# Kernel optimization log

Measured on AMD Instinct MI355X. Metric: run time of the kernel, lower is better.

Reference implementation:

```python
import jax, jax.numpy as jnp
import numpy as np

B, N, C, H = 8, 512, 64, 128
T, K = 10, 2                       # dilation threshold and skip divisor
TAUS = (0.25, 0.5, 0.75)
WTS = (0.25, 0.5, 0.25)
EPS_GIN = 0.0                      # (1 + eps) * x, eps buffer
AVG_DEG = 32.0


def setup_inputs() -> dict:
    key = jax.random.key(0)
    ks = jax.random.split(key, 6)
    x = jax.random.normal(ks[0], (B, N, C), jnp.float32)
    u = jax.random.uniform(ks[1], (B, N, N))
    a = u < (AVG_DEG / N)
    adj = jnp.maximum(a, jnp.swapaxes(a, 1, 2)).astype(jnp.float32)  # symmetric binary adjacency
    mask = jax.random.bernoulli(ks[2], 0.9, (B, N))
    W1 = jax.random.normal(ks[3], (C, H), jnp.float32) / np.float32(np.sqrt(C))
    b1 = jnp.zeros((H,), jnp.float32)
    W2 = jax.random.normal(ks[4], (H, C), jnp.float32) / np.float32(np.sqrt(H))
    b2 = jnp.zeros((C,), jnp.float32)
    return {"x": x, "adj": adj, "mask": mask, "W1": W1, "b1": b1, "W2": W2, "b2": b2}


def reference(x, adj, mask, W1, b1, W2, b2):
    Bc, Nc, Cc = x.shape
    eye = jnp.eye(Nc, dtype=bool)
    adj_ = jnp.where(eye, 1.0, adj)                 # add_loop=True: force self loops
    # ---- vectorized dilation (replaces the per-(b,n) python loop) ----
    neigh = (adj_ > 0) & (~eye)                     # neighbors excluding self [B,N,N]
    ni = neigh.astype(jnp.int32)
    rank = jnp.cumsum(ni, axis=-1) - ni             # exclusive rank of m among n's sorted neighbors
    nb = ni.sum(-1)                                 # [B,N] neighbor count (w/o self)
    skip = jnp.where(nb > T, (nb + K - 1) // K, 1)  # ceil(nb/k) if nb > T else 1 (linear mode, layer 1)
    skip = jnp.maximum(skip, 1)
    sk = skip[:, :, None]
    # remove relative indices skip-1, 2*skip-1, ... when skip > 1, only for masked-in nodes
    rem = neigh & (sk > 1) & ((rank % sk) == (sk - 1)) & mask[:, :, None]
    rem = rem | jnp.swapaxes(rem, 1, 2)             # symmetric removal
    adj_d = jnp.where(rem, 0.0, adj_)
    # ---- masked quantile aggregation over neighbors (== nanquantile) ----
    nd = adj_d > 0                                  # includes self loop -> at least 1 valid
    vals = jnp.where(nd[..., None], x[:, None, :, :], jnp.inf)  # [B,N,M,C]; invalid -> +inf
    s = jnp.sort(vals, axis=2)                      # valid values first, ascending
    nv = nd.sum(2)                                  # [B,N] valid count per node
    agg = jnp.zeros_like(x)
    for tau, w in zip(TAUS, WTS):                   # small fixed loop over quantiles
        pos = jnp.asarray(tau, x.dtype) * jnp.maximum(nv - 1, 0).astype(x.dtype)
        lo = jnp.floor(pos).astype(jnp.int32)
        hi = jnp.ceil(pos).astype(jnp.int32)
        frac = (pos - lo.astype(x.dtype))[..., None]
        idx_lo = jnp.broadcast_to(lo[:, :, None, None], (Bc, Nc, 1, Cc))
        idx_hi = jnp.broadcast_to(hi[:, :, None, None], (Bc, Nc, 1, Cc))
        v_lo = jnp.take_along_axis(s, idx_lo, axis=2)[:, :, 0, :]
        v_hi = jnp.take_along_axis(s, idx_hi, axis=2)[:, :, 0, :]
        agg = agg + jnp.asarray(w, x.dtype) * (v_lo + frac * (v_hi - v_lo))
    agg = jnp.where(nv[..., None] > 0, agg, 0.0)    # nan_to_num for empty rows
    out = (1.0 + EPS_GIN) * x + agg
    h = jax.nn.relu(out @ W1 + b1)                  # GIN MLP: Linear-ReLU-Linear
    y = h @ W2 + b2
    return y * mask[..., None].astype(y.dtype)
```

## Files before the change

kernel.cpp:

```cpp
#include <hip/hip_runtime.h>
#include <cstdint>

#define B_ 8
#define N_ 512
#define C_ 64
#define H_ 128
#define T_ 10
#define K_ 2
#define WPR 16
#define NVMAX 96
#define TT 8
#define KS4 25

__device__ inline uint32_t fkey(float v) {
    uint32_t bits = __float_as_uint(v);
    return (bits & 0x80000000u) ? ~bits : (bits | 0x80000000u);
}
__device__ inline float fdec(uint32_t key) {
    uint32_t ok = (key & 0xFFFFFF00u) | 0x80u;
    uint32_t bits = (ok & 0x80000000u) ? (ok ^ 0x80000000u) : ~ok;
    return __uint_as_float(bits);
}

__global__ __launch_bounds__(256) void pass1_keep(const float* __restrict__ adj,
                                                  const int* __restrict__ mask,
                                                  uint32_t* __restrict__ keepbits) {
    int wid = threadIdx.x >> 6, lane = threadIdx.x & 63;
    int row = blockIdx.x * 4 + wid;
    int i = row & (N_ - 1);
    const float4* arow4 = (const float4*)(adj + (size_t)row * N_);
    float4 a0 = arow4[lane * 2];
    float4 a1 = arow4[lane * 2 + 1];
    float av[8] = {a0.x, a0.y, a0.z, a0.w, a1.x, a1.y, a1.z, a1.w};

    int flags = 0, cnt = 0;
    int jbase = lane * 8;
#pragma unroll
    for (int k = 0; k < 8; ++k) {
        int j = jbase + k;
        bool ng = (j != i) && (av[k] > 0.0f);
        flags |= ((int)ng) << k;
        cnt += (int)ng;
    }
    int inc = cnt;
#pragma unroll
    for (int d = 1; d < 64; d <<= 1) {
        int o = __shfl_up(inc, d, 64);
        if (lane >= d) inc += o;
    }
    int excl = inc - cnt;
    int nb = __shfl(inc, 63, 64);
    int skip = (nb > T_) ? ((nb + K_ - 1) / K_) : 1;
    if (skip < 1) skip = 1;
    int maski = mask[row];

    unsigned remb = 0;
    if (skip > 1 && maski != 0) {
        int r = excl;
#pragma unroll
        for (int k = 0; k < 8; ++k) {
            if ((flags >> k) & 1) {
                if (r % skip == skip - 1) remb |= 1u << k;
                ++r;
            }
        }
    }
    unsigned diagb = (i >= jbase && i < jbase + 8) ? (1u << (i - jbase)) : 0u;
    unsigned keepb = (((unsigned)flags | diagb) & ~remb) & 0xFFu;

    unsigned p0 = __shfl((int)keepb, (lane & 15) * 4 + 0, 64);
    unsigned p1 = __shfl((int)keepb, (lane & 15) * 4 + 1, 64);
    unsigned p2 = __shfl((int)keepb, (lane & 15) * 4 + 2, 64);
    unsigned p3 = __shfl((int)keepb, (lane & 15) * 4 + 3, 64);
    if (lane < WPR) {
        uint32_t w = (p0 & 0xFFu) | ((p1 & 0xFFu) << 8) |
                     ((p2 & 0xFFu) << 16) | ((p3 & 0xFFu) << 24);
        keepbits[(size_t)row * WPR + lane] = w;
    }
}

__global__ __launch_bounds__(256) void pass2_quant_mlp(
        const float* __restrict__ x,
        const int* __restrict__ mask, const uint32_t* __restrict__ keepbits,
        const float* __restrict__ W1, const float* __restrict__ b1,
        const float* __restrict__ W2, const float* __restrict__ b2,
        float* __restrict__ out) {
    int row = blockIdx.x;
    int b = row >> 9, i = row & (N_ - 1);
    int tid = threadIdx.x;
    int lane = tid & 63;
    int q = tid >> 6;

    __shared__ uint4 keysT4[C_ * KS4];
    __shared__ unsigned short kept[NVMAX];
    __shared__ int s_cnt;
    __shared__ float selv[6][C_];
    __shared__ int s_rr[6];
    __shared__ float s_frac[3];
    __shared__ float out_node[C_];
    __shared__ float hbuf[H_];

    if (tid == 0) s_cnt = 0;
    __syncthreads();

    const uint32_t* wrow  = keepbits + (size_t)row * WPR;
    const uint32_t* wbase = keepbits + (size_t)(b * N_) * WPR;

    for (int jb = 0; jb < N_; jb += 256) {
        int j = jb + tid;
        uint32_t aw = wrow[j >> 5];
        bool keep = (aw >> (j & 31)) & 1u;
        if (keep && j != i) {
            uint32_t tw = wbase[(size_t)j * WPR + (i >> 5)];
            keep = (tw >> (i & 31)) & 1u;
        }
        unsigned long long bal = __ballot(keep);
        int base = 0;
        if (lane == 0 && bal) base = atomicAdd(&s_cnt, __popcll(bal));
        base = __shfl(base, 0, 64);
        if (keep) {
            int pos = __popcll(bal & ((1ull << lane) - 1ull));
            int p = base + pos;
            if (p < NVMAX) kept[p] = (unsigned short)j;
        }
    }
    __syncthreads();
    int nv = s_cnt;
    if (nv > NVMAX) nv = NVMAX;
    int nvp = (nv + 3) & ~3;

    const float* xb = x + (size_t)b * N_ * C_;

    for (int t0 = q * 4; t0 < nvp; t0 += 16) {
        uint32_t kk[4];
#pragma unroll
        for (int e = 0; e < 4; ++e) {
            int t = t0 + e;
            uint32_t kv = 0xFFFFFFFFu;
            if (t < nv) {
                float v = xb[(size_t)kept[t] * C_ + lane];
                kv = (fkey(v) & 0xFFFFFF00u) | (uint32_t)t;
            }
            kk[e] = kv;
        }
        keysT4[lane * KS4 + (t0 >> 2)] = make_uint4(kk[0], kk[1], kk[2], kk[3]);
    }

    if (tid == 0) {
        const float taus[3] = {0.25f, 0.5f, 0.75f};
        float nm1 = (float)((nv - 1 > 0) ? nv - 1 : 0);
        for (int qq = 0; qq < 3; ++qq) {
            float pos = taus[qq] * nm1;
            int lo = (int)floorf(pos);
            int hi = (int)ceilf(pos);
            s_rr[2 * qq] = lo; s_rr[2 * qq + 1] = hi;
            s_frac[qq] = pos - (float)lo;
        }
    }
    __syncthreads();

    int rr0 = s_rr[0], rr1 = s_rr[1], rr2 = s_rr[2],
        rr3 = s_rr[3], rr4 = s_rr[4], rr5 = s_rr[5];

    const uint4* col = &keysT4[lane * KS4];
    int iters = nvp >> 2;

    for (int base = 0; base < nvp; base += 32) {
        int tbase = base + q * TT;
        if (tbase >= nvp) continue;
        uint4 ka = col[(tbase >> 2)];
        uint4 kb = col[(tbase >> 2) + 1];
        uint32_t k[TT] = {ka.x, ka.y, ka.z, ka.w, kb.x, kb.y, kb.z, kb.w};
        int ra[TT], rb[TT];
#pragma unroll
        for (int m = 0; m < TT; ++m) {
            if (tbase + m >= nv) k[m] = 0xFFFFFFFFu;
            ra[m] = 0; rb[m] = 0;
        }
#pragma unroll 2
        for (int it = 0; it < iters; ++it) {
            uint4 w = col[it];
#pragma unroll
            for (int m = 0; m < TT; ++m) {
                ra[m] += (int)(w.x < k[m]);
                rb[m] += (int)(w.y < k[m]);
                ra[m] += (int)(w.z < k[m]);
                rb[m] += (int)(w.w < k[m]);
            }
        }
#pragma unroll
        for (int m = 0; m < TT; ++m) {
            int rs = ra[m] + rb[m];
            bool h0 = rs == rr0, h1 = rs == rr1, h2 = rs == rr2;
            bool h3 = rs == rr3, h4 = rs == rr4, h5 = rs == rr5;
            if (h0 | h1 | h2 | h3 | h4 | h5) {
                float fv = fdec(k[m]);
                if (h0) selv[0][lane] = fv;
                if (h1) selv[1][lane] = fv;
                if (h2) selv[2][lane] = fv;
                if (h3) selv[3][lane] = fv;
                if (h4) selv[4][lane] = fv;
                if (h5) selv[5][lane] = fv;
            }
        }
    }
    __syncthreads();

    if (tid < C_) {
        float f0 = s_frac[0], f1 = s_frac[1], f2 = s_frac[2];
        float agg = 0.25f * (selv[0][tid] + f0 * (selv[1][tid] - selv[0][tid]));
        agg      += 0.5f  * (selv[2][tid] + f1 * (selv[3][tid] - selv[2][tid]));
        agg      += 0.25f * (selv[4][tid] + f2 * (selv[5][tid] - selv[4][tid]));
        out_node[tid] = xb[(size_t)i * C_ + tid] + agg;
    }
    __syncthreads();

    float maskf = (mask[row] != 0) ? 1.0f : 0.0f;
    if (tid < H_) {
        float acc = b1[tid];
        for (int c = 0; c < C_; ++c) acc += out_node[c] * W1[c * H_ + tid];
        hbuf[tid] = acc > 0.0f ? acc : 0.0f;
    }
    __syncthreads();
    if (tid < C_) {
        float acc = b2[tid];
        for (int k2 = 0; k2 < H_; ++k2) acc += hbuf[k2] * W2[k2 * C_ + tid];
        out[(size_t)row * C_ + tid] = acc * maskf;
    }
}

extern "C" void kernel_launch(void* const* d_in, const int* in_sizes, int n_in,
                              void* d_out, int out_size, void* d_ws, size_t ws_size,
                              hipStream_t stream) {
    const float* x   = (const float*)d_in[0];
    const float* adj = (const float*)d_in[1];
    const int*  mask = (const int*)d_in[2];
    const float* W1  = (const float*)d_in[3];
    const float* b1  = (const float*)d_in[4];
    const float* W2  = (const float*)d_in[5];
    const float* b2  = (const float*)d_in[6];
    float* out = (float*)d_out;

    uint32_t* keepbits = (uint32_t*)d_ws;

    hipLaunchKernelGGL(pass1_keep, dim3(B_ * N_ / 4), dim3(256), 0, stream,
                       adj, mask, keepbits);
    hipLaunchKernelGGL(pass2_quant_mlp, dim3(B_ * N_), dim3(256), 0, stream,
                       x, mask, keepbits, W1, b1, W2, b2, out);
}
```

Measured before the change: 171.0 us.

## Rotate LDS key layout, use inline-asm compare-accumulate, split MLP across all threads

The LDS key column stride drops to 24 uint4s, and each lane's slot index is rotated by lane&7 so the 16-byte rows no longer collide on banks. The rank-counting loop is split in two to follow that rotation. Its compare/add pairs become inline-asm v_cmp_lt_u32 + v_addc_co_u32, so each comparison feeds its carry straight into the add without extra select instructions. The two MLP matvecs now use all 256 threads with split-K partial sums, reusing the key buffer as scratch in place of separate shared arrays. The asm ties up eight SGPR pairs per call and adds scheduling constraints and register pressure.

```diff
diff --git a/kernel.cpp b/kernel.cpp
--- a/kernel.cpp
+++ b/kernel.cpp
@@ -10,7 +10,7 @@
 #define WPR 16
 #define NVMAX 96
 #define TT 8
-#define KS4 25
+#define KS4 24
 
 __device__ inline uint32_t fkey(float v) {
     uint32_t bits = __float_as_uint(v);
@@ -20,6 +20,37 @@
     uint32_t ok = (key & 0xFFFFFF00u) | 0x80u;
     uint32_t bits = (ok & 0x80000000u) ? (ok ^ 0x80000000u) : ~ok;
     return __uint_as_float(bits);
+}
+
+__device__ __forceinline__ void cmpacc8(uint32_t w,
+        uint32_t k0, uint32_t k1, uint32_t k2, uint32_t k3,
+        uint32_t k4, uint32_t k5, uint32_t k6, uint32_t k7,
+        int& r0, int& r1, int& r2, int& r3,
+        int& r4, int& r5, int& r6, int& r7) {
+    uint64_t c0, c1, c2, c3, c4, c5, c6, c7;
+    asm("v_cmp_lt_u32 %[c0], %[w], %[k0]\n\t"
+        "v_cmp_lt_u32 %[c1], %[w], %[k1]\n\t"
+        "v_cmp_lt_u32 %[c2], %[w], %[k2]\n\t"
+        "v_cmp_lt_u32 %[c3], %[w], %[k3]\n\t"
+        "v_cmp_lt_u32 %[c4], %[w], %[k4]\n\t"
+        "v_cmp_lt_u32 %[c5], %[w], %[k5]\n\t"
+        "v_cmp_lt_u32 %[c6], %[w], %[k6]\n\t"
+        "v_cmp_lt_u32 %[c7], %[w], %[k7]\n\t"
+        "v_addc_co_u32 %[r0], %[c0], 0, %[r0], %[c0]\n\t"
+        "v_addc_co_u32 %[r1], %[c1], 0, %[r1], %[c1]\n\t"
+        "v_addc_co_u32 %[r2], %[c2], 0, %[r2], %[c2]\n\t"
+        "v_addc_co_u32 %[r3], %[c3], 0, %[r3], %[c3]\n\t"
+        "v_addc_co_u32 %[r4], %[c4], 0, %[r4], %[c4]\n\t"
+        "v_addc_co_u32 %[r5], %[c5], 0, %[r5], %[c5]\n\t"
+        "v_addc_co_u32 %[r6], %[c6], 0, %[r6], %[c6]\n\t"
+        "v_addc_co_u32 %[r7], %[c7], 0, %[r7], %[c7]"
+        : [c0]"=s"(c0), [c1]"=s"(c1), [c2]"=s"(c2), [c3]"=s"(c3),
+          [c4]"=s"(c4), [c5]"=s"(c5), [c6]"=s"(c6), [c7]"=s"(c7),
+          [r0]"+v"(r0), [r1]"+v"(r1), [r2]"+v"(r2), [r3]"+v"(r3),
+          [r4]"+v"(r4), [r5]"+v"(r5), [r6]"+v"(r6), [r7]"+v"(r7)
+        : [w]"v"(w),
+          [k0]"v"(k0), [k1]"v"(k1), [k2]"v"(k2), [k3]"v"(k3),
+          [k4]"v"(k4), [k5]"v"(k5), [k6]"v"(k6), [k7]"v"(k7));
 }
 
 __global__ __launch_bounds__(256) void pass1_keep(const float* __restrict__ adj,
@@ -97,8 +128,7 @@
     __shared__ float selv[6][C_];
     __shared__ int s_rr[6];
     __shared__ float s_frac[3];
-    __shared__ float out_node[C_];
-    __shared__ float hbuf[H_];
+    float* mlp_buf = (float*)keysT4;
 
     if (tid == 0) s_cnt = 0;
     __syncthreads();
@@ -130,6 +160,7 @@
     int nvp = (nv + 3) & ~3;
 
     const float* xb = x + (size_t)b * N_ * C_;
+    int rot = lane & 7;
 
     for (int t0 = q * 4; t0 < nvp; t0 += 16) {
         uint32_t kk[4];
@@ -143,7 +174,8 @@
             }
             kk[e] = kv;
         }
-        keysT4[lane * KS4 + (t0 >> 2)] = make_uint4(kk[0], kk[1], kk[2], kk[3]);
+        int sb = (t0 >> 2) + rot; if (sb >= KS4) sb -= KS4;
+        keysT4[lane * KS4 + sb] = make_uint4(kk[0], kk[1], kk[2], kk[3]);
     }
 
     if (tid == 0) {
@@ -168,31 +200,42 @@
     for (int base = 0; base < nvp; base += 32) {
         int tbase = base + q * TT;
         if (tbase >= nvp) continue;
-        uint4 ka = col[(tbase >> 2)];
-        uint4 kb = col[(tbase >> 2) + 1];
+        int jb0 = tbase >> 2;
+        int s0 = jb0 + rot;     if (s0 >= KS4) s0 -= KS4;
+        int s1 = jb0 + 1 + rot; if (s1 >= KS4) s1 -= KS4;
+        uint4 ka = col[s0];
+        uint4 kb = col[s1];
         uint32_t k[TT] = {ka.x, ka.y, ka.z, ka.w, kb.x, kb.y, kb.z, kb.w};
-        int ra[TT], rb[TT];
+        int r0 = 0, r1 = 0, r2 = 0, r3 = 0, r4 = 0, r5 = 0, r6 = 0, r7 = 0;
+#pragma unroll
+        for (int m = 0; m < TT; ++m)
+            if (tbase + m >= nv) k[m] = 0xFFFFFFFFu;
+
+        int n1 = KS4 - rot; if (n1 > iters) n1 = iters;
+#pragma unroll 2
+        for (int j = 0; j < n1; ++j) {
+            uint4 w = col[rot + j];
+            cmpacc8(w.x, k[0],k[1],k[2],k[3],k[4],k[5],k[6],k[7], r0,r1,r2,r3,r4,r5,r6,r7);
+            cmpacc8(w.y, k[0],k[1],k[2],k[3],k[4],k[5],k[6],k[7], r0,r1,r2,r3,r4,r5,r6,r7);
+            cmpacc8(w.z, k[0],k[1],k[2],k[3],k[4],k[5],k[6],k[7], r0,r1,r2,r3,r4,r5,r6,r7);
+            cmpacc8(w.w, k[0],k[1],k[2],k[3],k[4],k[5],k[6],k[7], r0,r1,r2,r3,r4,r5,r6,r7);
+        }
+        int n2 = iters - n1;
+#pragma unroll 2
+        for (int j = 0; j < n2; ++j) {
+            uint4 w = col[j];
+            cmpacc8(w.x, k[0],k[1],k[2],k[3],k[4],k[5],k[6],k[7], r0,r1,r2,r3,r4,r5,r6,r7);
+            cmpacc8(w.y, k[0],k[1],k[2],k[3],k[4],k[5],k[6],k[7], r0,r1,r2,r3,r4,r5,r6,r7);
+            cmpacc8(w.z, k[0],k[1],k[2],k[3],k[4],k[5],k[6],k[7], r0,r1,r2,r3,r4,r5,r6,r7);
+            cmpacc8(w.w, k[0],k[1],k[2],k[3],k[4],k[5],k[6],k[7], r0,r1,r2,r3,r4,r5,r6,r7);
+        }
+
+        int rs[TT] = {r0, r1, r2, r3, r4, r5, r6, r7};
 #pragma unroll
         for (int m = 0; m < TT; ++m) {
-            if (tbase + m >= nv) k[m] = 0xFFFFFFFFu;
-            ra[m] = 0; rb[m] = 0;
-        }
-#pragma unroll 2
-        for (int it = 0; it < iters; ++it) {
-            uint4 w = col[it];
-#pragma unroll
-            for (int m = 0; m < TT; ++m) {
-                ra[m] += (int)(w.x < k[m]);
-                rb[m] += (int)(w.y < k[m]);
-                ra[m] += (int)(w.z < k[m]);
-                rb[m] += (int)(w.w < k[m]);
-            }
-        }
-#pragma unroll
-        for (int m = 0; m < TT; ++m) {
-            int rs = ra[m] + rb[m];
-            bool h0 = rs == rr0, h1 = rs == rr1, h2 = rs == rr2;
-            bool h3 = rs == rr3, h4 = rs == rr4, h5 = rs == rr5;
+            int r = rs[m];
+            bool h0 = r == rr0, h1 = r == rr1, h2 = r == rr2;
+            bool h3 = r == rr3, h4 = r == rr4, h5 = r == rr5;
             if (h0 | h1 | h2 | h3 | h4 | h5) {
                 float fv = fdec(k[m]);
                 if (h0) selv[0][lane] = fv;
@@ -211,21 +254,43 @@
         float agg = 0.25f * (selv[0][tid] + f0 * (selv[1][tid] - selv[0][tid]));
         agg      += 0.5f  * (selv[2][tid] + f1 * (selv[3][tid] - selv[2][tid]));
         agg      += 0.25f * (selv[4][tid] + f2 * (selv[5][tid] - selv[4][tid]));
-        out_node[tid] = xb[(size_t)i * C_ + tid] + agg;
-    }
-    __syncthreads();
-
-    float maskf = (mask[row] != 0) ? 1.0f : 0.0f;
+        mlp_buf[tid] = xb[(size_t)i * C_ + tid] + agg;
+    }
+    __syncthreads();
+
+    {
+        int hcol = tid & 127, chalf = tid >> 7;
+        float acc = 0.0f;
+#pragma unroll 4
+        for (int c = 0; c < 32; ++c) {
+            int c0 = chalf * 32 + c;
+            acc += mlp_buf[c0] * W1[c0 * H_ + hcol];
+        }
+        mlp_buf[192 + tid] = acc;
+    }
+    __syncthreads();
     if (tid < H_) {
-        float acc = b1[tid];
-        for (int c = 0; c < C_; ++c) acc += out_node[c] * W1[c * H_ + tid];
-        hbuf[tid] = acc > 0.0f ? acc : 0.0f;
+        float h = mlp_buf[192 + tid] + mlp_buf[192 + tid + 128] + b1[tid];
+        mlp_buf[64 + tid] = h > 0.0f ? h : 0.0f;
+    }
+    __syncthreads();
+
+    {
+        int ycol = tid & 63, kq = tid >> 6;
+        float acc = 0.0f;
+#pragma unroll 4
+        for (int kk = 0; kk < 32; ++kk) {
+            int k0 = kq * 32 + kk;
+            acc += mlp_buf[64 + k0] * W2[k0 * C_ + ycol];
+        }
+        mlp_buf[192 + tid] = acc;
     }
     __syncthreads();
     if (tid < C_) {
-        float acc = b2[tid];
-        for (int k2 = 0; k2 < H_; ++k2) acc += hbuf[k2] * W2[k2 * C_ + tid];
-        out[(size_t)row * C_ + tid] = acc * maskf;
+        float maskf = (mask[row] != 0) ? 1.0f : 0.0f;
+        float y = b2[tid] + mlp_buf[192 + tid] + mlp_buf[192 + tid + 64]
+                + mlp_buf[192 + tid + 128] + mlp_buf[192 + tid + 192];
+        out[(size_t)row * C_ + tid] = y * maskf;
     }
 }
 
```

Result: slower. 175.9 us (+2.9%).
